# Optimization experiments

Measured on AMD Instinct MI355X. Metric: run time of the kernel, lower is better.

## Reference

```python
import jax, jax.numpy as jnp
import numpy as np

N = 50000
E = 800000
DIMS = [(8, 16), (16, 16), (16, 16)]  # (in, out) per layer


def setup_inputs() -> dict:
    key = jax.random.key(0)
    ks = jax.random.split(key, 32)
    inp = {}
    inp['x'] = jax.random.normal(ks[0], (N, 8), dtype=jnp.float32)
    inp['pos'] = jax.random.normal(ks[1], (N, 3), dtype=jnp.float32)
    k = 2
    for i, (ci, co) in enumerate(DIMS):
        d = ci * co
        inp[f'lin_w{i}'] = jax.random.normal(ks[k], (3, d), dtype=jnp.float32); k += 1
        inp[f'lin_b{i}'] = jax.random.normal(ks[k], (d,), dtype=jnp.float32); k += 1
        inp[f'gamma{i}'] = jax.random.normal(ks[k], (d,), dtype=jnp.float32); k += 1
        inp[f'beta{i}'] = jax.random.normal(ks[k], (d,), dtype=jnp.float32); k += 1
        inp[f'root{i}'] = jax.random.normal(ks[k], (ci, co), dtype=jnp.float32); k += 1
        inp[f'bias{i}'] = jax.random.normal(ks[k], (co,), dtype=jnp.float32); k += 1
    inp['batch'] = jnp.zeros((N,), dtype=jnp.int32)
    inp['idx'] = jnp.sort(jax.random.randint(ks[k], (25000,), 0, N, dtype=jnp.int32)); k += 1
    inp['edge_index'] = jax.random.randint(ks[k], (2, E), 0, N, dtype=jnp.int32)
    return inp


def _nnconv(x, pseudo, src, dst, lin_w, lin_b, gamma, beta, root, bias, ci, co):
    # edge MLP (Linear -> batchnorm(eval, affine) -> ReLU), plain_last=False
    w = jax.nn.relu((pseudo @ lin_w + lin_b) * gamma + beta)  # [E, ci*co]
    w = w.reshape(-1, ci, co)                                  # [E, ci, co]
    msg = jnp.einsum('ei,eio->eo', x[src], w)                  # per-edge vec-mat
    s = jax.ops.segment_sum(msg, dst, num_segments=N)          # scatter-sum
    cnt = jax.ops.segment_sum(jnp.ones((msg.shape[0],), x.dtype), dst, num_segments=N)
    aggr = s / jnp.maximum(cnt, 1.0)[:, None]                  # scatter-mean
    return aggr + x @ root + bias


def reference(x, pos, lin_w0, lin_b0, gamma0, beta0, root0, bias0,
              lin_w1, lin_b1, gamma1, beta1, root1, bias1,
              lin_w2, lin_b2, gamma2, beta2, root2, bias2,
              batch, idx, edge_index):
    src, dst = edge_index[0], edge_index[1]
    pseudo = pos[dst] - pos[src]  # patch_size is None
    params = [
        (lin_w0, lin_b0, gamma0, beta0, root0, bias0),
        (lin_w1, lin_b1, gamma1, beta1, root1, bias1),
        (lin_w2, lin_b2, gamma2, beta2, root2, bias2),
    ]
    h = x
    for (ci, co), p in zip(DIMS, params):
        h = jax.nn.relu(_nnconv(h, pseudo, src, dst, *p, ci, co))  # drop_act=False
    return h[idx], pos[idx], batch[idx]
```

## Files before the change

### kernel.cpp

```cpp
#include <hip/hip_runtime.h>

#define N_NODES 50000
#define N_EDGES 800000
#define M_IDX   25000

template<int CI>
__global__ __launch_bounds__(256) void edge_kernel(
    const float* __restrict__ pos,
    const int*   __restrict__ src,
    const int*   __restrict__ dst,
    const float* __restrict__ h,
    const float* __restrict__ lin_w,
    const float* __restrict__ lin_b,
    const float* __restrict__ gamma,
    const float* __restrict__ beta,
    float*       __restrict__ aggr,
    int E)
{
    const int o = threadIdx.x & 15;
    const int d = CI * 16;
    float W0[CI], W1[CI], W2[CI], B[CI];
#pragma unroll
    for (int i = 0; i < CI; ++i) {
        int j = i * 16 + o;
        float g = gamma[j];
        W0[i] = lin_w[j] * g;
        W1[i] = lin_w[d + j] * g;
        W2[i] = lin_w[2 * d + j] * g;
        B[i]  = fmaf(lin_b[j], g, beta[j]);
    }
    const int group   = (blockIdx.x * blockDim.x + threadIdx.x) >> 4;
    const int ngroups = (gridDim.x * blockDim.x) >> 4;
    for (int e = group; e < E; e += ngroups) {
        const int s = src[e];
        const int t = dst[e];
        const float p0 = pos[t * 3 + 0] - pos[s * 3 + 0];
        const float p1 = pos[t * 3 + 1] - pos[s * 3 + 1];
        const float p2 = pos[t * 3 + 2] - pos[s * 3 + 2];
        float x[CI];
        const float4* xp = (const float4*)(h + (size_t)s * CI);
#pragma unroll
        for (int q = 0; q < CI / 4; ++q) {
            float4 v = xp[q];
            x[4 * q + 0] = v.x; x[4 * q + 1] = v.y;
            x[4 * q + 2] = v.z; x[4 * q + 3] = v.w;
        }
        float msg = 0.f;
#pragma unroll
        for (int i = 0; i < CI; ++i) {
            float w = fmaf(p2, W2[i], fmaf(p1, W1[i], fmaf(p0, W0[i], B[i])));
            w = fmaxf(w, 0.f);
            msg = fmaf(x[i], w, msg);
        }
        atomicAdd(&aggr[(size_t)t * 16 + o], msg);
    }
}

__global__ __launch_bounds__(256) void count_kernel(
    const int* __restrict__ dst, int* __restrict__ cnt, int E)
{
    int e = blockIdx.x * blockDim.x + threadIdx.x;
    if (e < E) atomicAdd(&cnt[dst[e]], 1);
}

template<int CI>
__global__ __launch_bounds__(256) void node_kernel(
    const float* __restrict__ aggr,
    const int*   __restrict__ cnt,
    const float* __restrict__ h_in,
    const float* __restrict__ root,
    const float* __restrict__ bias,
    float*       __restrict__ h_out,
    int N)
{
    int t = blockIdx.x * blockDim.x + threadIdx.x;
    if (t >= N * 16) return;
    int n = t >> 4, o = t & 15;
    float c = (float)cnt[n];
    float inv = 1.0f / fmaxf(c, 1.0f);
    float acc = fmaf(aggr[t], inv, bias[o]);
#pragma unroll
    for (int i = 0; i < CI; ++i)
        acc = fmaf(h_in[(size_t)n * CI + i], root[i * 16 + o], acc);
    h_out[t] = fmaxf(acc, 0.f);
}

__global__ __launch_bounds__(256) void gather_kernel(
    const float* __restrict__ h,
    const float* __restrict__ pos,
    const int*   __restrict__ batch,
    const int*   __restrict__ idx,
    float*       __restrict__ out,
    int M)
{
    int j = blockIdx.x * blockDim.x + threadIdx.x;
    if (j >= M) return;
    int n = idx[j];
    float4*       o4 = (float4*)out + (size_t)j * 4;
    const float4* h4 = (const float4*)(h + (size_t)n * 16);
    o4[0] = h4[0]; o4[1] = h4[1]; o4[2] = h4[2]; o4[3] = h4[3];
    float* po = out + (size_t)M * 16 + (size_t)j * 3;
    po[0] = pos[n * 3 + 0];
    po[1] = pos[n * 3 + 1];
    po[2] = pos[n * 3 + 2];
    ((int*)out)[(size_t)M * 19 + j] = batch[n];
}

extern "C" void kernel_launch(void* const* d_in, const int* in_sizes, int n_in,
                              void* d_out, int out_size, void* d_ws, size_t ws_size,
                              hipStream_t stream) {
    const float* x      = (const float*)d_in[0];
    const float* pos    = (const float*)d_in[1];
    const float* lin_w0 = (const float*)d_in[2];
    const float* lin_b0 = (const float*)d_in[3];
    const float* gamma0 = (const float*)d_in[4];
    const float* beta0  = (const float*)d_in[5];
    const float* root0  = (const float*)d_in[6];
    const float* bias0  = (const float*)d_in[7];
    const float* lin_w1 = (const float*)d_in[8];
    const float* lin_b1 = (const float*)d_in[9];
    const float* gamma1 = (const float*)d_in[10];
    const float* beta1  = (const float*)d_in[11];
    const float* root1  = (const float*)d_in[12];
    const float* bias1  = (const float*)d_in[13];
    const float* lin_w2 = (const float*)d_in[14];
    const float* lin_b2 = (const float*)d_in[15];
    const float* gamma2 = (const float*)d_in[16];
    const float* beta2  = (const float*)d_in[17];
    const float* root2  = (const float*)d_in[18];
    const float* bias2  = (const float*)d_in[19];
    const int*   batch  = (const int*)d_in[20];
    const int*   idx    = (const int*)d_in[21];
    const int*   ei     = (const int*)d_in[22];
    const int*   src    = ei;
    const int*   dst    = ei + N_EDGES;
    float*       out    = (float*)d_out;

    float* aggr = (float*)d_ws;
    float* hA   = aggr + (size_t)N_NODES * 16;
    float* hB   = hA   + (size_t)N_NODES * 16;
    int*   cnt  = (int*)(hB + (size_t)N_NODES * 16);

    const int EB = 2048;
    const int NB = (N_NODES * 16 + 255) / 256;

    hipMemsetAsync(cnt, 0, N_NODES * sizeof(int), stream);
    count_kernel<<<(N_EDGES + 255) / 256, 256, 0, stream>>>(dst, cnt, N_EDGES);

    hipMemsetAsync(aggr, 0, (size_t)N_NODES * 16 * sizeof(float), stream);
    edge_kernel<8><<<EB, 256, 0, stream>>>(pos, src, dst, x,
                                           lin_w0, lin_b0, gamma0, beta0,
                                           aggr, N_EDGES);
    node_kernel<8><<<NB, 256, 0, stream>>>(aggr, cnt, x, root0, bias0, hA, N_NODES);

    hipMemsetAsync(aggr, 0, (size_t)N_NODES * 16 * sizeof(float), stream);
    edge_kernel<16><<<EB, 256, 0, stream>>>(pos, src, dst, hA,
                                            lin_w1, lin_b1, gamma1, beta1,
                                            aggr, N_EDGES);
    node_kernel<16><<<NB, 256, 0, stream>>>(aggr, cnt, hA, root1, bias1, hB, N_NODES);

    hipMemsetAsync(aggr, 0, (size_t)N_NODES * 16 * sizeof(float), stream);
    edge_kernel<16><<<EB, 256, 0, stream>>>(pos, src, dst, hB,
                                            lin_w2, lin_b2, gamma2, beta2,
                                            aggr, N_EDGES);
    node_kernel<16><<<NB, 256, 0, stream>>>(aggr, cnt, hB, root2, bias2, hA, N_NODES);

    gather_kernel<<<(M_IDX + 255) / 256, 256, 0, stream>>>(hA, pos, batch, idx, out, M_IDX);
}
```

Before: 346.4 us.

## Replace atomic scatter with a CSR-like pull aggregation fused into the node update

After: 414.5 us. 1.2x slower.

```diff
diff --git a/kernel.cpp b/kernel.cpp
--- a/kernel.cpp
+++ b/kernel.cpp
@@ -3,19 +3,33 @@
 #define N_NODES 50000
 #define N_EDGES 800000
 #define M_IDX   25000
+#define ADJ_STRIDE 64
+
+__global__ __launch_bounds__(256) void build_adj_kernel(
+    const int* __restrict__ src, const int* __restrict__ dst,
+    int* __restrict__ cnt, int* __restrict__ adj, int E)
+{
+    int e = blockIdx.x * blockDim.x + threadIdx.x;
+    if (e >= E) return;
+    int t = dst[e];
+    int p = atomicAdd(&cnt[t], 1);
+    if (p < ADJ_STRIDE) adj[t * ADJ_STRIDE + p] = src[e];
+}
 
 template<int CI>
-__global__ __launch_bounds__(256) void edge_kernel(
+__global__ __launch_bounds__(256) void aggr_node_kernel(
     const float* __restrict__ pos,
-    const int*   __restrict__ src,
-    const int*   __restrict__ dst,
-    const float* __restrict__ h,
+    const int*   __restrict__ adj,
+    const int*   __restrict__ cnt,
+    const float* __restrict__ h_in,
     const float* __restrict__ lin_w,
     const float* __restrict__ lin_b,
     const float* __restrict__ gamma,
     const float* __restrict__ beta,
-    float*       __restrict__ aggr,
-    int E)
+    const float* __restrict__ root,
+    const float* __restrict__ bias,
+    float*       __restrict__ h_out,
+    int nNodes)
 {
     const int o = threadIdx.x & 15;
     const int d = CI * 16;
@@ -29,60 +43,71 @@
         W2[i] = lin_w[2 * d + j] * g;
         B[i]  = fmaf(lin_b[j], g, beta[j]);
     }
+    const float bo = bias[o];
+
     const int group   = (blockIdx.x * blockDim.x + threadIdx.x) >> 4;
     const int ngroups = (gridDim.x * blockDim.x) >> 4;
-    for (int e = group; e < E; e += ngroups) {
-        const int s = src[e];
-        const int t = dst[e];
-        const float p0 = pos[t * 3 + 0] - pos[s * 3 + 0];
-        const float p1 = pos[t * 3 + 1] - pos[s * 3 + 1];
-        const float p2 = pos[t * 3 + 2] - pos[s * 3 + 2];
-        float x[CI];
-        const float4* xp = (const float4*)(h + (size_t)s * CI);
+    for (int t = group; t < nNodes; t += ngroups) {
+        const int deg  = cnt[t];
+        const int base = t * ADJ_STRIDE;
+        const float pt0 = pos[t * 3 + 0];
+        const float pt1 = pos[t * 3 + 1];
+        const float pt2 = pos[t * 3 + 2];
+
+        float acc = 0.f;
+        float pn0 = 0.f, pn1 = 0.f, pn2 = 0.f;
+        float xn[CI];
+#pragma unroll
+        for (int i = 0; i < CI; ++i) xn[i] = 0.f;
+        if (deg > 0) {
+            int s = adj[base];
+            pn0 = pos[s * 3 + 0]; pn1 = pos[s * 3 + 1]; pn2 = pos[s * 3 + 2];
+            const float4* xp = (const float4*)(h_in + (size_t)s * CI);
+#pragma unroll
+            for (int q = 0; q < CI / 4; ++q) {
+                float4 v = xp[q];
+                xn[4 * q + 0] = v.x; xn[4 * q + 1] = v.y;
+                xn[4 * q + 2] = v.z; xn[4 * q + 3] = v.w;
+            }
+        }
+        for (int p = 0; p < deg; ++p) {
+            const float p0 = pt0 - pn0;
+            const float p1 = pt1 - pn1;
+            const float p2 = pt2 - pn2;
+            float xc[CI];
+#pragma unroll
+            for (int i = 0; i < CI; ++i) xc[i] = xn[i];
+            if (p + 1 < deg) {
+                int s = adj[base + p + 1];
+                pn0 = pos[s * 3 + 0]; pn1 = pos[s * 3 + 1]; pn2 = pos[s * 3 + 2];
+                const float4* xp = (const float4*)(h_in + (size_t)s * CI);
+#pragma unroll
+                for (int q = 0; q < CI / 4; ++q) {
+                    float4 v = xp[q];
+                    xn[4 * q + 0] = v.x; xn[4 * q + 1] = v.y;
+                    xn[4 * q + 2] = v.z; xn[4 * q + 3] = v.w;
+                }
+            }
+#pragma unroll
+            for (int i = 0; i < CI; ++i) {
+                float w = fmaf(p2, W2[i], fmaf(p1, W1[i], fmaf(p0, W0[i], B[i])));
+                w = fmaxf(w, 0.f);
+                acc = fmaf(xc[i], w, acc);
+            }
+        }
+        const float inv = 1.0f / fmaxf((float)deg, 1.0f);
+        float r = fmaf(acc, inv, bo);
+        const float4* hp = (const float4*)(h_in + (size_t)t * CI);
 #pragma unroll
         for (int q = 0; q < CI / 4; ++q) {
-            float4 v = xp[q];
-            x[4 * q + 0] = v.x; x[4 * q + 1] = v.y;
-            x[4 * q + 2] = v.z; x[4 * q + 3] = v.w;
+            float4 v = hp[q];
+            r = fmaf(v.x, root[(4 * q + 0) * 16 + o], r);
+            r = fmaf(v.y, root[(4 * q + 1) * 16 + o], r);
+            r = fmaf(v.z, root[(4 * q + 2) * 16 + o], r);
+            r = fmaf(v.w, root[(4 * q + 3) * 16 + o], r);
         }
-        float msg = 0.f;
-#pragma unroll
-        for (int i = 0; i < CI; ++i) {
-            float w = fmaf(p2, W2[i], fmaf(p1, W1[i], fmaf(p0, W0[i], B[i])));
-            w = fmaxf(w, 0.f);
-            msg = fmaf(x[i], w, msg);
-        }
-        atomicAdd(&aggr[(size_t)t * 16 + o], msg);
+        h_out[(size_t)t * 16 + o] = fmaxf(r, 0.f);
     }
-}
-
-__global__ __launch_bounds__(256) void count_kernel(
-    const int* __restrict__ dst, int* __restrict__ cnt, int E)
-{
-    int e = blockIdx.x * blockDim.x + threadIdx.x;
-    if (e < E) atomicAdd(&cnt[dst[e]], 1);
-}
-
-template<int CI>
-__global__ __launch_bounds__(256) void node_kernel(
-    const float* __restrict__ aggr,
-    const int*   __restrict__ cnt,
-    const float* __restrict__ h_in,
-    const float* __restrict__ root,
-    const float* __restrict__ bias,
-    float*       __restrict__ h_out,
-    int N)
-{
-    int t = blockIdx.x * blockDim.x + threadIdx.x;
-    if (t >= N * 16) return;
-    int n = t >> 4, o = t & 15;
-    float c = (float)cnt[n];
-    float inv = 1.0f / fmaxf(c, 1.0f);
-    float acc = fmaf(aggr[t], inv, bias[o]);
-#pragma unroll
-    for (int i = 0; i < CI; ++i)
-        acc = fmaf(h_in[(size_t)n * CI + i], root[i * 16 + o], acc);
-    h_out[t] = fmaxf(acc, 0.f);
 }
 
 __global__ __launch_bounds__(256) void gather_kernel(
@@ -136,34 +161,22 @@
     const int*   dst    = ei + N_EDGES;
     float*       out    = (float*)d_out;
 
-    float* aggr = (float*)d_ws;
-    float* hA   = aggr + (size_t)N_NODES * 16;
-    float* hB   = hA   + (size_t)N_NODES * 16;
-    int*   cnt  = (int*)(hB + (size_t)N_NODES * 16);
+    int*   adj = (int*)d_ws;
+    float* hA  = (float*)(adj + (size_t)N_NODES * ADJ_STRIDE);
+    float* hB  = hA + (size_t)N_NODES * 16;
+    int*   cnt = (int*)(hB + (size_t)N_NODES * 16);
 
-    const int EB = 2048;
-    const int NB = (N_NODES * 16 + 255) / 256;
+    const int AGG_BLOCKS = 1024;
 
     hipMemsetAsync(cnt, 0, N_NODES * sizeof(int), stream);
-    count_kernel<<<(N_EDGES + 255) / 256, 256, 0, stream>>>(dst, cnt, N_EDGES);
+    build_adj_kernel<<<(N_EDGES + 255) / 256, 256, 0, stream>>>(src, dst, cnt, adj, N_EDGES);
 
-    hipMemsetAsync(aggr, 0, (size_t)N_NODES * 16 * sizeof(float), stream);
-    edge_kernel<8><<<EB, 256, 0, stream>>>(pos, src, dst, x,
-                                           lin_w0, lin_b0, gamma0, beta0,
-                                           aggr, N_EDGES);
-    node_kernel<8><<<NB, 256, 0, stream>>>(aggr, cnt, x, root0, bias0, hA, N_NODES);
-
-    hipMemsetAsync(aggr, 0, (size_t)N_NODES * 16 * sizeof(float), stream);
-    edge_kernel<16><<<EB, 256, 0, stream>>>(pos, src, dst, hA,
-                                            lin_w1, lin_b1, gamma1, beta1,
-                                            aggr, N_EDGES);
-    node_kernel<16><<<NB, 256, 0, stream>>>(aggr, cnt, hA, root1, bias1, hB, N_NODES);
-
-    hipMemsetAsync(aggr, 0, (size_t)N_NODES * 16 * sizeof(float), stream);
-    edge_kernel<16><<<EB, 256, 0, stream>>>(pos, src, dst, hB,
-                                            lin_w2, lin_b2, gamma2, beta2,
-                                            aggr, N_EDGES);
-    node_kernel<16><<<NB, 256, 0, stream>>>(aggr, cnt, hB, root2, bias2, hA, N_NODES);
+    aggr_node_kernel<8><<<AGG_BLOCKS, 256, 0, stream>>>(
+        pos, adj, cnt, x, lin_w0, lin_b0, gamma0, beta0, root0, bias0, hA, N_NODES);
+    aggr_node_kernel<16><<<AGG_BLOCKS, 256, 0, stream>>>(
+        pos, adj, cnt, hA, lin_w1, lin_b1, gamma1, beta1, root1, bias1, hB, N_NODES);
+    aggr_node_kernel<16><<<AGG_BLOCKS, 256, 0, stream>>>(
+        pos, adj, cnt, hB, lin_w2, lin_b2, gamma2, beta2, root2, bias2, hA, N_NODES);
 
     gather_kernel<<<(M_IDX + 255) / 256, 256, 0, stream>>>(hA, pos, batch, idx, out, M_IDX);
 }
```

## Build dst-sorted CSR edge list and fuse edge aggregation with node update

Applied to the files above, without the earlier changes.

New measurement: 426.9 us. 1.23x slower.

```diff
diff --git a/kernel.cpp b/kernel.cpp
--- a/kernel.cpp
+++ b/kernel.cpp
@@ -3,20 +3,98 @@
 #define N_NODES 50000
 #define N_EDGES 800000
 #define M_IDX   25000
+#define G_NODES 32
+#define SCAN_B  256
+
+__global__ __launch_bounds__(256) void hist_kernel(
+    const int* __restrict__ dst, int* __restrict__ cnt, int E)
+{
+    int e = blockIdx.x * blockDim.x + threadIdx.x;
+    if (e < E) atomicAdd(&cnt[dst[e]], 1);
+}
+
+__global__ __launch_bounds__(SCAN_B) void scan1_kernel(
+    const int* __restrict__ cnt, int* __restrict__ off,
+    int* __restrict__ bsum, int N)
+{
+    __shared__ int sh[SCAN_B];
+    int i = blockIdx.x * SCAN_B + threadIdx.x;
+    int v = (i < N) ? cnt[i] : 0;
+    sh[threadIdx.x] = v;
+    __syncthreads();
+    for (int d = 1; d < SCAN_B; d <<= 1) {
+        int t = (threadIdx.x >= d) ? sh[threadIdx.x - d] : 0;
+        __syncthreads();
+        sh[threadIdx.x] += t;
+        __syncthreads();
+    }
+    if (i < N) off[i] = sh[threadIdx.x] - v;
+    if (threadIdx.x == SCAN_B - 1) bsum[blockIdx.x] = sh[threadIdx.x];
+}
+
+__global__ __launch_bounds__(SCAN_B) void scan2_kernel(int* __restrict__ bsum, int nb)
+{
+    __shared__ int sh[SCAN_B];
+    int v = (threadIdx.x < nb) ? bsum[threadIdx.x] : 0;
+    sh[threadIdx.x] = v;
+    __syncthreads();
+    for (int d = 1; d < SCAN_B; d <<= 1) {
+        int t = (threadIdx.x >= d) ? sh[threadIdx.x - d] : 0;
+        __syncthreads();
+        sh[threadIdx.x] += t;
+        __syncthreads();
+    }
+    if (threadIdx.x < nb) bsum[threadIdx.x] = sh[threadIdx.x] - v;
+}
+
+__global__ __launch_bounds__(SCAN_B) void scan3_kernel(
+    int* __restrict__ off, const int* __restrict__ bsum,
+    int* __restrict__ cursor, int N)
+{
+    int i = blockIdx.x * SCAN_B + threadIdx.x;
+    if (i < N) {
+        int o = off[i] + bsum[blockIdx.x];
+        off[i] = o;
+        cursor[i] = o;
+    }
+}
+
+__global__ __launch_bounds__(256) void fill_kernel(
+    const int*   __restrict__ ei,
+    const float* __restrict__ pos,
+    int*         __restrict__ cursor,
+    float4*      __restrict__ pp,
+    int E)
+{
+    int e = blockIdx.x * blockDim.x + threadIdx.x;
+    if (e >= E) return;
+    int s = ei[e];
+    int t = ei[E + e];
+    float4 pd;
+    pd.x = pos[t * 3 + 0] - pos[s * 3 + 0];
+    pd.y = pos[t * 3 + 1] - pos[s * 3 + 1];
+    pd.z = pos[t * 3 + 2] - pos[s * 3 + 2];
+    pd.w = __int_as_float(s | (t << 16));
+    int slot = atomicAdd(&cursor[t], 1);
+    pp[slot] = pd;
+}
 
 template<int CI>
-__global__ __launch_bounds__(256) void edge_kernel(
-    const float* __restrict__ pos,
-    const int*   __restrict__ src,
-    const int*   __restrict__ dst,
-    const float* __restrict__ h,
-    const float* __restrict__ lin_w,
-    const float* __restrict__ lin_b,
-    const float* __restrict__ gamma,
-    const float* __restrict__ beta,
-    float*       __restrict__ aggr,
-    int E)
-{
+__global__ __launch_bounds__(256) void fused_layer_kernel(
+    const float4* __restrict__ pp,
+    const int*    __restrict__ off,
+    const int*    __restrict__ cnt,
+    const float*  __restrict__ h_in,
+    const float*  __restrict__ lin_w,
+    const float*  __restrict__ lin_b,
+    const float*  __restrict__ gamma,
+    const float*  __restrict__ beta,
+    const float*  __restrict__ root,
+    const float*  __restrict__ bias,
+    float*        __restrict__ h_out,
+    int N, int E)
+{
+    __shared__ float sacc[G_NODES * 16];
     const int o = threadIdx.x & 15;
     const int d = CI * 16;
     float W0[CI], W1[CI], W2[CI], B[CI];
@@ -29,60 +107,65 @@
         W2[i] = lin_w[2 * d + j] * g;
         B[i]  = fmaf(lin_b[j], g, beta[j]);
     }
-    const int group   = (blockIdx.x * blockDim.x + threadIdx.x) >> 4;
-    const int ngroups = (gridDim.x * blockDim.x) >> 4;
-    for (int e = group; e < E; e += ngroups) {
-        const int s = src[e];
-        const int t = dst[e];
-        const float p0 = pos[t * 3 + 0] - pos[s * 3 + 0];
-        const float p1 = pos[t * 3 + 1] - pos[s * 3 + 1];
-        const float p2 = pos[t * 3 + 2] - pos[s * 3 + 2];
-        float x[CI];
-        const float4* xp = (const float4*)(h + (size_t)s * CI);
+    const int n0 = blockIdx.x * G_NODES;
+    for (int i = threadIdx.x; i < G_NODES * 16; i += 256) sacc[i] = 0.f;
+    __syncthreads();
+
+    const int s0 = off[n0];
+    const int s1 = (n0 + G_NODES >= N) ? E : off[n0 + G_NODES];
+    const int grp = threadIdx.x >> 4;
+
+    for (int slot = s0 + grp; slot < s1; slot += 32) {
+        const int slotB = slot + 16;
+        const bool vB = (slotB < s1);
+        float4 pdA = pp[slot];
+        float4 pdB = vB ? pp[slotB] : pdA;
+        const int pkA = __float_as_int(pdA.w);
+        const int pkB = __float_as_int(pdB.w);
+        const int sA = pkA & 0xFFFF, tA = ((unsigned)pkA) >> 16;
+        const int sB = pkB & 0xFFFF, tB = ((unsigned)pkB) >> 16;
+        float xA[CI], xB[CI];
+        const float4* xpA = (const float4*)(h_in + (size_t)sA * CI);
+        const float4* xpB = (const float4*)(h_in + (size_t)sB * CI);
 #pragma unroll
         for (int q = 0; q < CI / 4; ++q) {
-            float4 v = xp[q];
-            x[4 * q + 0] = v.x; x[4 * q + 1] = v.y;
-            x[4 * q + 2] = v.z; x[4 * q + 3] = v.w;
+            float4 a = xpA[q];
+            xA[4 * q + 0] = a.x; xA[4 * q + 1] = a.y;
+            xA[4 * q + 2] = a.z; xA[4 * q + 3] = a.w;
+            float4 b = xpB[q];
+            xB[4 * q + 0] = b.x; xB[4 * q + 1] = b.y;
+            xB[4 * q + 2] = b.z; xB[4 * q + 3] = b.w;
         }
-        float msg = 0.f;
+        float aA = 0.f, aB = 0.f;
 #pragma unroll
         for (int i = 0; i < CI; ++i) {
-            float w = fmaf(p2, W2[i], fmaf(p1, W1[i], fmaf(p0, W0[i], B[i])));
-            w = fmaxf(w, 0.f);
-            msg = fmaf(x[i], w, msg);
+            float wA = fmaf(pdA.z, W2[i], fmaf(pdA.y, W1[i], fmaf(pdA.x, W0[i], B[i])));
+            aA = fmaf(xA[i], fmaxf(wA, 0.f), aA);
+            float wB = fmaf(pdB.z, W2[i], fmaf(pdB.y, W1[i], fmaf(pdB.x, W0[i], B[i])));
+            aB = fmaf(xB[i], fmaxf(wB, 0.f), aB);
         }
-        atomicAdd(&aggr[(size_t)t * 16 + o], msg);
-    }
-}
-
-__global__ __launch_bounds__(256) void count_kernel(
-    const int* __restrict__ dst, int* __restrict__ cnt, int E)
-{
-    int e = blockIdx.x * blockDim.x + threadIdx.x;
-    if (e < E) atomicAdd(&cnt[dst[e]], 1);
-}
-
-template<int CI>
-__global__ __launch_bounds__(256) void node_kernel(
-    const float* __restrict__ aggr,
-    const int*   __restrict__ cnt,
-    const float* __restrict__ h_in,
-    const float* __restrict__ root,
-    const float* __restrict__ bias,
-    float*       __restrict__ h_out,
-    int N)
-{
-    int t = blockIdx.x * blockDim.x + threadIdx.x;
-    if (t >= N * 16) return;
-    int n = t >> 4, o = t & 15;
-    float c = (float)cnt[n];
-    float inv = 1.0f / fmaxf(c, 1.0f);
-    float acc = fmaf(aggr[t], inv, bias[o]);
-#pragma unroll
-    for (int i = 0; i < CI; ++i)
-        acc = fmaf(h_in[(size_t)n * CI + i], root[i * 16 + o], acc);
-    h_out[t] = fmaxf(acc, 0.f);
+        atomicAdd(&sacc[(tA - n0) * 16 + o], aA);
+        if (vB) atomicAdd(&sacc[(tB - n0) * 16 + o], aB);
+    }
+    __syncthreads();
+
+    for (int i = threadIdx.x; i < G_NODES * 16; i += 256) {
+        int n = n0 + (i >> 4);
+        if (n >= N) continue;
+        int oc = i & 15;
+        float deg = (float)cnt[n];
+        float r = fmaf(sacc[i], 1.0f / fmaxf(deg, 1.0f), bias[oc]);
+        const float4* hp = (const float4*)(h_in + (size_t)n * CI);
+#pragma unroll
+        for (int q = 0; q < CI / 4; ++q) {
+            float4 v = hp[q];
+            r = fmaf(v.x, root[(4 * q + 0) * 16 + oc], r);
+            r = fmaf(v.y, root[(4 * q + 1) * 16 + oc], r);
+            r = fmaf(v.z, root[(4 * q + 2) * 16 + oc], r);
+            r = fmaf(v.w, root[(4 * q + 3) * 16 + oc], r);
+        }
+        h_out[(size_t)n * 16 + oc] = fmaxf(r, 0.f);
+    }
 }
 
 __global__ __launch_bounds__(256) void gather_kernel(
@@ -132,38 +215,33 @@
     const int*   batch  = (const int*)d_in[20];
     const int*   idx    = (const int*)d_in[21];
     const int*   ei     = (const int*)d_in[22];
-    const int*   src    = ei;
     const int*   dst    = ei + N_EDGES;
     float*       out    = (float*)d_out;
 
-    float* aggr = (float*)d_ws;
-    float* hA   = aggr + (size_t)N_NODES * 16;
-    float* hB   = hA   + (size_t)N_NODES * 16;
-    int*   cnt  = (int*)(hB + (size_t)N_NODES * 16);
-
-    const int EB = 2048;
-    const int NB = (N_NODES * 16 + 255) / 256;
+    float4* pp     = (float4*)d_ws;
+    float*  hA     = (float*)(pp + N_EDGES);
+    float*  hB     = hA + (size_t)N_NODES * 16;
+    int*    cnt    = (int*)(hB + (size_t)N_NODES * 16);
+    int*    off    = cnt + N_NODES;
+    int*    cursor = off + N_NODES;
+    int*    bsum   = cursor + N_NODES;
+
+    const int SCAN_BLOCKS  = (N_NODES + SCAN_B - 1) / SCAN_B;
+    const int FUSED_BLOCKS = (N_NODES + G_NODES - 1) / G_NODES;
 
     hipMemsetAsync(cnt, 0, N_NODES * sizeof(int), stream);
-    count_kernel<<<(N_EDGES + 255) / 256, 256, 0, stream>>>(dst, cnt, N_EDGES);
-
-    hipMemsetAsync(aggr, 0, (size_t)N_NODES * 16 * sizeof(float), stream);
-    edge_kernel<8><<<EB, 256, 0, stream>>>(pos, src, dst, x,
-                                           lin_w0, lin_b0, gamma0, beta0,
-                                           aggr, N_EDGES);
-    node_kernel<8><<<NB, 256, 0, stream>>>(aggr, cnt, x, root0, bias0, hA, N_NODES);
-
-    hipMemsetAsync(aggr, 0, (size_t)N_NODES * 16 * sizeof(float), stream);
-    edge_kernel<16><<<EB, 256, 0, stream>>>(pos, src, dst, hA,
-                                            lin_w1, lin_b1, gamma1, beta1,
-                                            aggr, N_EDGES);
-    node_kernel<16><<<NB, 256, 0, stream>>>(aggr, cnt, hA, root1, bias1, hB, N_NODES);
-
-    hipMemsetAsync(aggr, 0, (size_t)N_NODES * 16 * sizeof(float), stream);
-    edge_kernel<16><<<EB, 256, 0, stream>>>(pos, src, dst, hB,
-                                            lin_w2, lin_b2, gamma2, beta2,
-                                            aggr, N_EDGES);
-    node_kernel<16><<<NB, 256, 0, stream>>>(aggr, cnt, hB, root2, bias2, hA, N_NODES);
+    hist_kernel<<<(N_EDGES + 255) / 256, 256, 0, stream>>>(dst, cnt, N_EDGES);
+    scan1_kernel<<<SCAN_BLOCKS, SCAN_B, 0, stream>>>(cnt, off, bsum, N_NODES);
+    scan2_kernel<<<1, SCAN_B, 0, stream>>>(bsum, SCAN_BLOCKS);
+    scan3_kernel<<<SCAN_BLOCKS, SCAN_B, 0, stream>>>(off, bsum, cursor, N_NODES);
+    fill_kernel<<<(N_EDGES + 255) / 256, 256, 0, stream>>>(ei, pos, cursor, pp, N_EDGES);
+
+    fused_layer_kernel<8><<<FUSED_BLOCKS, 256, 0, stream>>>(
+        pp, off, cnt, x, lin_w0, lin_b0, gamma0, beta0, root0, bias0, hA, N_NODES, N_EDGES);
+    fused_layer_kernel<16><<<FUSED_BLOCKS, 256, 0, stream>>>(
+        pp, off, cnt, hA, lin_w1, lin_b1, gamma1, beta1, root1, bias1, hB, N_NODES, N_EDGES);
+    fused_layer_kernel<16><<<FUSED_BLOCKS, 256, 0, stream>>>(
+        pp, off, cnt, hB, lin_w2, lin_b2, gamma2, beta2, root2, bias2, hA, N_NODES, N_EDGES);
 
     gather_kernel<<<(M_IDX + 255) / 256, 256, 0, stream>>>(hA, pos, batch, idx, out, M_IDX);
 }
```
